# Kernel optimization log

Hardware: AMD Instinct MI355X
Metric: run time of the kernel (lower is better)

Reference implementation:

```python
import jax, jax.numpy as jnp
import numpy as np

N_ENEMY = 4_000_000
N_GUN = 1_000_000
N_EDGES = 16_000_000
HID = 64
OUT = 8


def setup_inputs() -> dict:
    key = jax.random.key(0)
    ks = jax.random.split(key, 9)
    x_enemy = jax.random.normal(ks[0], (N_ENEMY, 4), dtype=jnp.float32)
    x_gun = jax.random.normal(ks[1], (N_GUN, 1), dtype=jnp.float32)
    edge_src = jax.random.randint(ks[2], (N_EDGES,), 0, N_ENEMY, dtype=jnp.int64 if jax.config.jax_enable_x64 else jnp.int32)
    edge_dst = jax.random.randint(ks[3], (N_EDGES,), 0, N_GUN, dtype=jnp.int64 if jax.config.jax_enable_x64 else jnp.int32)
    W_l = jax.random.normal(ks[4], (4, HID), dtype=jnp.float32) * 0.5
    b_l = jax.random.normal(ks[5], (HID,), dtype=jnp.float32) * 0.1
    W_r = jax.random.normal(ks[6], (1, HID), dtype=jnp.float32) * 0.5
    W_fc = jax.random.normal(ks[7], (HID, OUT), dtype=jnp.float32) * 0.1
    b_fc = jax.random.normal(ks[8], (OUT,), dtype=jnp.float32) * 0.1
    return {"x_enemy": x_enemy, "x_gun": x_gun, "edge_src": edge_src,
            "edge_dst": edge_dst, "W_l": W_l, "b_l": b_l, "W_r": W_r,
            "W_fc": W_fc, "b_fc": b_fc}


def reference(x_enemy, x_gun, edge_src, edge_dst, W_l, b_l, W_r, W_fc, b_fc):
    n_gun = x_gun.shape[0]
    # gather enemy messages along edges: [E, 4]
    msgs = x_enemy[edge_src]
    # mean aggregation per gun node (zero for isolated nodes, like PyG scatter-mean)
    summed = jax.ops.segment_sum(msgs, edge_dst, num_segments=n_gun)  # [N_gun, 4]
    counts = jax.ops.segment_sum(jnp.ones((edge_dst.shape[0],), dtype=x_enemy.dtype),
                                 edge_dst, num_segments=n_gun)       # [N_gun]
    mean = summed / jnp.maximum(counts, 1.0)[:, None]
    # SAGEConv: lin_l(aggr) + lin_r(x_dst)  (lin_l has bias, lin_r bias-free)
    h = mean @ W_l + b_l + x_gun @ W_r                                # [N_gun, HID]
    # linear head -> q values
    return h @ W_fc + b_fc                                            # [N_gun, OUT]
```

## Files before the change

### kernel.cpp

```cpp
#include <hip/hip_runtime.h>

#define N_ENEMY 4000000
#define N_GUN   1000000
#define N_EDGES 16000000
#define OUTD    8

#define NB   1024
#define GPB  977
#define T8   8192
#define NT8  1954
#define EPT8 32

#define CH   4096
#define CEPT 16

#define NS   8
#define SEG_CAP 16128

__device__ __forceinline__ unsigned int bucket_of(unsigned int dst) {
    return (unsigned int)(((unsigned long long)dst * 1125395730ull) >> 40);
}
__device__ __forceinline__ unsigned int rne_bf16(unsigned int u) {
    return (u + 0x7FFFu + ((u >> 16) & 1u)) >> 16;
}
__device__ __forceinline__ unsigned int get_xcc() {
    unsigned int x;
    asm("s_getreg_b32 %0, hwreg(HW_REG_XCC_ID)" : "=s"(x));
    return x;
}

__global__ void prep_params(const float* __restrict__ W_l, const float* __restrict__ b_l,
                            const float* __restrict__ W_r, const float* __restrict__ W_fc,
                            const float* __restrict__ b_fc, float* __restrict__ P) {
    int o = threadIdx.x;
    if (o < OUTD) {
        float a0 = 0.f, a1 = 0.f, a2 = 0.f, a3 = 0.f, r = 0.f, c = 0.f;
        for (int h = 0; h < 64; ++h) {
            float w = W_fc[h * OUTD + o];
            a0 += W_l[0 * 64 + h] * w;
            a1 += W_l[1 * 64 + h] * w;
            a2 += W_l[2 * 64 + h] * w;
            a3 += W_l[3 * 64 + h] * w;
            r  += W_r[h] * w;
            c  += b_l[h] * w;
        }
        P[0 * OUTD + o] = a0;
        P[1 * OUTD + o] = a1;
        P[2 * OUTD + o] = a2;
        P[3 * OUTD + o] = a3;
        P[4 * OUTD + o] = r;
        P[5 * OUTD + o] = c + b_fc[o];
    }
}

__global__ void conv_kernel(const uint4* __restrict__ xe, uint2* __restrict__ xeb) {
    int i = blockIdx.x * blockDim.x + threadIdx.x;
    if (i >= N_ENEMY) return;
    uint4 v = xe[i];
    uint2 q;
    q.x = rne_bf16(v.x) | (rne_bf16(v.y) << 16);
    q.y = rne_bf16(v.z) | (rne_bf16(v.w) << 16);
    xeb[i] = q;
}

__global__ void hist2_kernel(const int* __restrict__ edst, unsigned short* __restrict__ tileh) {
    __shared__ unsigned int lh[NB];
    int t = threadIdx.x;
    for (int i = t; i < NB; i += 256) lh[i] = 0;
    __syncthreads();
    int ebase = blockIdx.x * T8;
    int nE = N_EDGES - ebase;
    if (nE > T8) nE = T8;
    for (int i = t; i < nE; i += 256)
        atomicAdd(&lh[bucket_of((unsigned)edst[ebase + i])], 1u);
    __syncthreads();
    unsigned short* row = tileh + (size_t)blockIdx.x * NB;
    for (int i = t; i < NB; i += 256) row[i] = (unsigned short)lh[i];
}

template<int K>
__global__ __launch_bounds__(256)
void tile_scanT(unsigned short* __restrict__ tileh, unsigned int* __restrict__ tot,
                int nbk, int ntile) {
    __shared__ unsigned int part[256][17];
    int t = threadIdx.x;
    int b0 = blockIdx.x * 16;
    unsigned int loc[16];
#pragma unroll
    for (int j = 0; j < 16; ++j) loc[j] = 0;
    for (int k = 0; k < K; ++k) {
        int tile = t * K + k;
        if (tile < ntile) {
            const unsigned short* row = tileh + (size_t)tile * nbk + b0;
#pragma unroll
            for (int j = 0; j < 16; ++j) loc[j] += row[j];
        }
    }
#pragma unroll
    for (int j = 0; j < 16; ++j) part[t][j] = loc[j];
    __syncthreads();
    if (t < 16) {
        unsigned int acc = 0;
        for (int i = 0; i < 256; ++i) {
            unsigned int v = part[i][t];
            part[i][t] = acc;
            acc += v;
        }
        tot[b0 + t] = acc;
    }
    __syncthreads();
    unsigned int run[16];
#pragma unroll
    for (int j = 0; j < 16; ++j) run[j] = part[t][j];
    for (int k = 0; k < K; ++k) {
        int tile = t * K + k;
        if (tile < ntile) {
            unsigned short* row = tileh + (size_t)tile * nbk + b0;
#pragma unroll
            for (int j = 0; j < 16; ++j) {
                unsigned int c = row[j];
                row[j] = (unsigned short)run[j];
                run[j] += c;
            }
        }
    }
}

__global__ void scan_kernel(const unsigned int* __restrict__ tot,
                            unsigned int* __restrict__ offsets) {
    __shared__ unsigned int tmp[1024];
    int t = threadIdx.x;
    unsigned int v0 = (t < NB) ? tot[t] : 0u;
    tmp[t] = v0;
    __syncthreads();
    for (int d = 1; d < 1024; d <<= 1) {
        unsigned int v = (t >= d) ? tmp[t - d] : 0u;
        __syncthreads();
        tmp[t] += v;
        __syncthreads();
    }
    if (t < NB) offsets[t] = tmp[t] - v0;
    if (t == NB - 1) offsets[NB] = tmp[t];
}

__global__ __launch_bounds__(256, 2)
void scatter_sorted(const int* __restrict__ esrc, const int* __restrict__ edst,
                    const unsigned int* __restrict__ offsets,
                    const unsigned short* __restrict__ tileh,
                    unsigned int* __restrict__ payload) {
    __shared__ unsigned int cnt[NB];
    __shared__ unsigned int base[NB];
    __shared__ unsigned int gb[NB];
    __shared__ unsigned short bOf[T8];
    __shared__ unsigned int sorted[T8];
    __shared__ unsigned int partial[256];
    int t = threadIdx.x;
    int tile = blockIdx.x;
    int ebase = tile * T8;
    int nE = N_EDGES - ebase;
    if (nE > T8) nE = T8;
    for (int i = t; i < NB; i += 256) cnt[i] = 0;
    __syncthreads();
    unsigned int w[EPT8];
    unsigned int br[EPT8];
#pragma unroll
    for (int k = 0; k < EPT8; ++k) {
        int idx = k * 256 + t;
        if (idx < nE) {
            unsigned int s = (unsigned int)esrc[ebase + idx];
            unsigned int d = (unsigned int)edst[ebase + idx];
            unsigned int b = bucket_of(d);
            unsigned int g = d - b * GPB;
            unsigned int r = atomicAdd(&cnt[b], 1u);
            w[k]  = (s << 10) | g;
            br[k] = (b << 13) | r;
        } else br[k] = 0xFFFFFFFFu;
    }
    __syncthreads();
    unsigned int loc[4];
    unsigned int s = 0;
#pragma unroll
    for (int j = 0; j < 4; ++j) {
        int b = t * 4 + j;
        unsigned int c = cnt[b];
        loc[j] = s; s += c;
    }
    partial[t] = s;
    __syncthreads();
    for (int d = 1; d < 256; d <<= 1) {
        unsigned int v = (t >= d) ? partial[t - d] : 0u;
        __syncthreads();
        partial[t] += v;
        __syncthreads();
    }
    unsigned int excl = (t > 0) ? partial[t - 1] : 0u;
#pragma unroll
    for (int j = 0; j < 4; ++j) base[t * 4 + j] = excl + loc[j];
    __syncthreads();
    const unsigned short* trow = tileh + (size_t)tile * NB;
#pragma unroll
    for (int j = 0; j < 4; ++j) {
        int b = t * 4 + j;
        gb[b] = offsets[b] + (unsigned int)trow[b];
        unsigned int bs = base[b];
        unsigned int c = cnt[b];
        for (unsigned int p = bs; p < bs + c; ++p) bOf[p] = (unsigned short)b;
    }
    __syncthreads();
#pragma unroll
    for (int k = 0; k < EPT8; ++k) {
        if (br[k] != 0xFFFFFFFFu) {
            unsigned int b = br[k] >> 13;
            unsigned int r = br[k] & 8191u;
            sorted[base[b] + r] = w[k];
        }
    }
    __syncthreads();
    for (int p = t; p < nE; p += 256) {
        unsigned int b = bOf[p];
        payload[gb[b] + ((unsigned int)p - base[b])] = sorted[p];
    }
}

__global__ __launch_bounds__(256)
void slice_sort(const unsigned int* __restrict__ offsets,
                unsigned int* __restrict__ payload,
                unsigned int* __restrict__ stab) {
    __shared__ unsigned int A[SEG_CAP];
    __shared__ unsigned int cnt[NS];
    __shared__ unsigned int base[NS + 1];
    int b = blockIdx.x;
    int t = threadIdx.x;
    unsigned int segS = offsets[b];
    unsigned int segE = offsets[b + 1];
    unsigned int len = segE - segS;
    if (len > SEG_CAP) {
        if (t <= NS) stab[b * (NS + 1) + t] = (t == 0) ? segS : segE;
        return;
    }
    if (t < NS) cnt[t] = 0;
    __syncthreads();
    for (unsigned int i = t; i < len; i += 256) {
        unsigned int w = payload[segS + i];
        A[i] = w;
        atomicAdd(&cnt[w >> 29], 1u);
    }
    __syncthreads();
    if (t == 0) {
        unsigned int acc = 0;
        for (int k = 0; k < NS; ++k) { base[k] = acc; acc += cnt[k]; }
        base[NS] = acc;
    }
    __syncthreads();
    if (t < NS) cnt[t] = 0;
    __syncthreads();
    for (unsigned int i = t; i < len; i += 256) {
        unsigned int w = A[i];
        unsigned int k = w >> 29;
        unsigned int r = atomicAdd(&cnt[k], 1u);
        payload[segS + base[k] + r] = w;
    }
    if (t <= NS) stab[b * (NS + 1) + t] = segS + base[t];
}

__global__ __launch_bounds__(256)
void bucket_v9(const unsigned int* __restrict__ stab,
               const unsigned int* __restrict__ payload,
               const uint2* __restrict__ xeb,
               const float* __restrict__ xg,
               const float* __restrict__ P,
               float* __restrict__ out) {
    __shared__ unsigned long long sorted[CH];
    __shared__ unsigned int cnt[1024];
    __shared__ unsigned int base_[1024];
    __shared__ unsigned int partial[256];
    __shared__ float sP[48];
    int t = threadIdx.x;
    if (t < 48) sP[t] = P[t];
    __syncthreads();

    float a0[4] = {0,0,0,0}, a1[4] = {0,0,0,0}, a2[4] = {0,0,0,0}, a3[4] = {0,0,0,0};
    float an[4] = {0,0,0,0};

    unsigned int b = blockIdx.x;
    unsigned int rot = get_xcc() & (NS - 1u);

    for (int si = 0; si < NS; ++si) {
        unsigned int s = ((unsigned int)si + rot) & (NS - 1u);
        unsigned int rs = stab[b * (NS + 1) + s];
        unsigned int re = stab[b * (NS + 1) + s + 1];

        for (unsigned int cs = rs; cs < re; cs += CH) {
            int n = (int)((re - cs < (unsigned int)CH) ? (re - cs) : (unsigned int)CH);
            for (int i = t; i < 1024; i += 256) cnt[i] = 0;
            __syncthreads();

            unsigned int g_[CEPT], r_[CEPT];
            uint2 q_[CEPT];
#pragma unroll
            for (int k = 0; k < CEPT; ++k) {
                int idx = k * 256 + t;
                if (idx < n) {
                    unsigned int p = payload[cs + idx];
                    q_[k] = xeb[p >> 10];
                    unsigned int g = p & 1023u;
                    g_[k] = g;
                    r_[k] = atomicAdd(&cnt[g], 1u);
                } else g_[k] = 0xFFFFFFFFu;
            }
            __syncthreads();

            unsigned int loc[4];
            unsigned int acc = 0;
#pragma unroll
            for (int j = 0; j < 4; ++j) {
                loc[j] = acc; acc += cnt[t * 4 + j];
            }
            partial[t] = acc;
            __syncthreads();
            for (int d = 1; d < 256; d <<= 1) {
                unsigned int v = (t >= d) ? partial[t - d] : 0u;
                __syncthreads();
                partial[t] += v;
                __syncthreads();
            }
            unsigned int excl = (t > 0) ? partial[t - 1] : 0u;
#pragma unroll
            for (int j = 0; j < 4; ++j) base_[t * 4 + j] = excl + loc[j];
            __syncthreads();

#pragma unroll
            for (int k = 0; k < CEPT; ++k) {
                if (g_[k] != 0xFFFFFFFFu) {
                    sorted[base_[g_[k]] + r_[k]] =
                        ((unsigned long long)q_[k].y << 32) | (unsigned long long)q_[k].x;
                }
            }
            __syncthreads();

#pragma unroll
            for (int j = 0; j < 4; ++j) {
                int g = j * 256 + t;
                unsigned int bs = base_[g], c = cnt[g];
                for (unsigned int p2 = bs; p2 < bs + c; ++p2) {
                    unsigned long long v = sorted[p2];
                    unsigned int lo = (unsigned int)v, hi = (unsigned int)(v >> 32);
                    a0[j] += __uint_as_float(lo << 16);
                    a1[j] += __uint_as_float(lo & 0xffff0000u);
                    a2[j] += __uint_as_float(hi << 16);
                    a3[j] += __uint_as_float(hi & 0xffff0000u);
                }
                an[j] += (float)c;
            }
            __syncthreads();
        }
    }

#pragma unroll
    for (int j = 0; j < 4; ++j) {
        int g = j * 256 + t;
        if (g >= GPB) continue;
        unsigned int G = b * GPB + (unsigned int)g;
        if (G >= N_GUN) continue;
        float inv = 1.0f / fmaxf(an[j], 1.0f);
        float m0 = a0[j] * inv, m1 = a1[j] * inv, m2 = a2[j] * inv, m3 = a3[j] * inv;
        float xv = xg[G];
        float res[OUTD];
#pragma unroll
        for (int o = 0; o < OUTD; ++o) {
            res[o] = m0 * sP[o] + m1 * sP[8 + o] + m2 * sP[16 + o] + m3 * sP[24 + o]
                   + xv * sP[32 + o] + sP[40 + o];
        }
        float4* op = (float4*)(out + (size_t)G * OUTD);
        op[0] = make_float4(res[0], res[1], res[2], res[3]);
        op[1] = make_float4(res[4], res[5], res[6], res[7]);
    }
}

__global__ void edge_kernel(const int4* __restrict__ esrc4, const int4* __restrict__ edst4,
                            const float4* __restrict__ xe, float* __restrict__ summed,
                            float* __restrict__ counts) {
    int t = blockIdx.x * blockDim.x + threadIdx.x;
    if (t >= N_EDGES / 4) return;
    int4 s4 = esrc4[t];
    int4 d4 = edst4[t];
    int ss[4] = { s4.x, s4.y, s4.z, s4.w };
    int dd[4] = { d4.x, d4.y, d4.z, d4.w };
#pragma unroll
    for (int k = 0; k < 4; ++k) {
        float4 m = xe[ss[k]];
        float* basep = summed + (size_t)dd[k] * 4;
        atomicAdd(basep + 0, m.x);
        atomicAdd(basep + 1, m.y);
        atomicAdd(basep + 2, m.z);
        atomicAdd(basep + 3, m.w);
        atomicAdd(counts + dd[k], 1.0f);
    }
}

__global__ void gun_kernel(const float4* __restrict__ summed, const float* __restrict__ counts,
                           const float* __restrict__ xg, const float* __restrict__ P,
                           float* __restrict__ out) {
    __shared__ float sP[48];
    if (threadIdx.x < 48) sP[threadIdx.x] = P[threadIdx.x];
    __syncthreads();
    int g = blockIdx.x * blockDim.x + threadIdx.x;
    if (g >= N_GUN) return;
    float4 s = summed[g];
    float cnt = counts[g];
    float inv = 1.0f / fmaxf(cnt, 1.0f);
    float m0 = s.x * inv, m1 = s.y * inv, m2 = s.z * inv, m3 = s.w * inv;
    float xv = xg[g];
    float res[OUTD];
#pragma unroll
    for (int o = 0; o < OUTD; ++o) {
        res[o] = m0 * sP[o] + m1 * sP[8 + o] + m2 * sP[16 + o] + m3 * sP[24 + o]
               + xv * sP[32 + o] + sP[40 + o];
    }
    float4* op = (float4*)(out + (size_t)g * OUTD);
    op[0] = make_float4(res[0], res[1], res[2], res[3]);
    op[1] = make_float4(res[4], res[5], res[6], res[7]);
}

extern "C" void kernel_launch(void* const* d_in, const int* in_sizes, int n_in,
                              void* d_out, int out_size, void* d_ws, size_t ws_size,
                              hipStream_t stream) {
    const float* x_enemy = (const float*)d_in[0];
    const float* x_gun   = (const float*)d_in[1];
    const int*   esrc    = (const int*)d_in[2];
    const int*   edst    = (const int*)d_in[3];
    const float* W_l     = (const float*)d_in[4];
    const float* b_l     = (const float*)d_in[5];
    const float* W_r     = (const float*)d_in[6];
    const float* W_fc    = (const float*)d_in[7];
    const float* b_fc    = (const float*)d_in[8];
    float* out = (float*)d_out;

    const size_t PAYLOAD_OFF = 0;
    const size_t XEB_OFF     = (size_t)N_EDGES;
    const size_t TOT_OFF     = XEB_OFF + (size_t)N_ENEMY*2;
    const size_t OFFS_OFF    = TOT_OFF + NB;
    const size_t P_OFF       = OFFS_OFF + NB + 1;
    const size_t STAB_OFF    = P_OFF + 48;
    const size_t NEEDED_FULL = (STAB_OFF + (size_t)NB * (NS + 1) + 16) * sizeof(unsigned int);

    if (ws_size >= NEEDED_FULL) {
        unsigned int*   ws      = (unsigned int*)d_ws;
        unsigned int*   payload = ws + PAYLOAD_OFF;
        uint2*          xeb     = (uint2*)(ws + XEB_OFF);
        unsigned short* tileh   = (unsigned short*)(ws + XEB_OFF);
        unsigned int*   tot     = ws + TOT_OFF;
        unsigned int*   offsets = ws + OFFS_OFF;
        float*          P       = (float*)(ws + P_OFF);
        unsigned int*   stab    = ws + STAB_OFF;

        prep_params<<<1, 64, 0, stream>>>(W_l, b_l, W_r, W_fc, b_fc, P);
        hist2_kernel<<<NT8, 256, 0, stream>>>(edst, tileh);
        tile_scanT<8><<<NB / 16, 256, 0, stream>>>(tileh, tot, NB, NT8);
        scan_kernel<<<1, 1024, 0, stream>>>(tot, offsets);
        scatter_sorted<<<NT8, 256, 0, stream>>>(esrc, edst, offsets, tileh, payload);
        slice_sort<<<NB, 256, 0, stream>>>(offsets, payload, stab);
        conv_kernel<<<(N_ENEMY + 255) / 256, 256, 0, stream>>>((const uint4*)x_enemy, xeb);
        bucket_v9<<<NB, 256, 0, stream>>>(stab, payload, xeb, x_gun, P, out);
    } else {
        float* summed = (float*)d_ws;
        float* counts = summed + (size_t)N_GUN * 4;
        float* P      = counts + N_GUN;
        hipMemsetAsync(d_ws, 0, ((size_t)N_GUN * 5 + 48) * sizeof(float), stream);
        prep_params<<<1, 64, 0, stream>>>(W_l, b_l, W_r, W_fc, b_fc, P);
        int edge_threads = N_EDGES / 4;
        edge_kernel<<<(edge_threads + 255) / 256, 256, 0, stream>>>(
            (const int4*)esrc, (const int4*)edst, (const float4*)x_enemy, summed, counts);
        gun_kernel<<<(N_GUN + 255) / 256, 256, 0, stream>>>(
            (const float4*)summed, counts, x_gun, P, out);
    }
}
```

Measured before the change: 413.5 us.

## Record in-tile ranks during histogram and use atomic-free slice sort

The histogram pass now stores each edge's within-tile bucket rank, a 16-bit value, so the scatter kernel can place edges directly without recomputing ranks through LDS atomics. The slice sort replaces shared-memory atomics with per-thread contiguous-range counting, a column prefix scan and deterministic placement. This adds a 32MB rank buffer that must be written and read back, and the workspace layout changes so that tileh no longer aliases xeb. The new path runs only if the workspace is large enough.

```diff
diff --git a/kernel.cpp b/kernel.cpp
--- a/kernel.cpp
+++ b/kernel.cpp
@@ -78,6 +78,24 @@
     for (int i = t; i < NB; i += 256) row[i] = (unsigned short)lh[i];
 }
 
+__global__ void hist3_kernel(const int* __restrict__ edst, unsigned short* __restrict__ tileh,
+                             unsigned short* __restrict__ rnk) {
+    __shared__ unsigned int lh[NB];
+    int t = threadIdx.x;
+    for (int i = t; i < NB; i += 256) lh[i] = 0;
+    __syncthreads();
+    int ebase = blockIdx.x * T8;
+    int nE = N_EDGES - ebase;
+    if (nE > T8) nE = T8;
+    for (int i = t; i < nE; i += 256) {
+        unsigned int b = bucket_of((unsigned)edst[ebase + i]);
+        rnk[ebase + i] = (unsigned short)atomicAdd(&lh[b], 1u);
+    }
+    __syncthreads();
+    unsigned short* row = tileh + (size_t)blockIdx.x * NB;
+    for (int i = t; i < NB; i += 256) row[i] = (unsigned short)lh[i];
+}
+
 template<int K>
 __global__ __launch_bounds__(256)
 void tile_scanT(unsigned short* __restrict__ tileh, unsigned int* __restrict__ tot,
@@ -222,13 +240,97 @@
     }
 }
 
+__global__ __launch_bounds__(256, 2)
+void scatter_nr(const int* __restrict__ esrc, const int* __restrict__ edst,
+                const unsigned short* __restrict__ rnk,
+                const unsigned int* __restrict__ offsets,
+                const unsigned short* __restrict__ tileh,
+                const unsigned int* __restrict__ tot,
+                unsigned int* __restrict__ payload) {
+    __shared__ unsigned int cnt[NB];
+    __shared__ unsigned int base[NB];
+    __shared__ unsigned int gb[NB];
+    __shared__ unsigned short bOf[T8];
+    __shared__ unsigned int sorted[T8];
+    __shared__ unsigned int partial[256];
+    int t = threadIdx.x;
+    int tile = blockIdx.x;
+    int ebase = tile * T8;
+    int nE = N_EDGES - ebase;
+    if (nE > T8) nE = T8;
+
+    const unsigned short* trow = tileh + (size_t)tile * NB;
+    const unsigned short* trowN = tileh + (size_t)(tile + 1) * NB;
+    unsigned int loc[4];
+    unsigned int s = 0;
+#pragma unroll
+    for (int j = 0; j < 4; ++j) {
+        int b = t * 4 + j;
+        unsigned int cur = trow[b];
+        unsigned int nxt = (tile == NT8 - 1) ? tot[b] : (unsigned int)trowN[b];
+        unsigned int c = nxt - cur;
+        cnt[b] = c;
+        gb[b] = offsets[b] + cur;
+        loc[j] = s; s += c;
+    }
+    partial[t] = s;
+    __syncthreads();
+    for (int d = 1; d < 256; d <<= 1) {
+        unsigned int v = (t >= d) ? partial[t - d] : 0u;
+        __syncthreads();
+        partial[t] += v;
+        __syncthreads();
+    }
+    unsigned int excl = (t > 0) ? partial[t - 1] : 0u;
+#pragma unroll
+    for (int j = 0; j < 4; ++j) base[t * 4 + j] = excl + loc[j];
+    __syncthreads();
+
+#pragma unroll
+    for (int j = 0; j < 4; ++j) {
+        int b = t * 4 + j;
+        unsigned int bs = base[b], c = cnt[b];
+        for (unsigned int p = bs; p < bs + c; ++p) bOf[p] = (unsigned short)b;
+    }
+
+    unsigned int w[EPT8], br[EPT8];
+#pragma unroll
+    for (int k = 0; k < EPT8; ++k) {
+        int idx = k * 256 + t;
+        if (idx < nE) {
+            unsigned int sv = (unsigned int)esrc[ebase + idx];
+            unsigned int d = (unsigned int)edst[ebase + idx];
+            unsigned int b = bucket_of(d);
+            unsigned int g = d - b * GPB;
+            unsigned int r = (unsigned int)rnk[ebase + idx];
+            w[k]  = (sv << 10) | g;
+            br[k] = (b << 13) | r;
+        } else br[k] = 0xFFFFFFFFu;
+    }
+    __syncthreads();
+
+#pragma unroll
+    for (int k = 0; k < EPT8; ++k) {
+        if (br[k] != 0xFFFFFFFFu) {
+            unsigned int b = br[k] >> 13;
+            unsigned int r = br[k] & 8191u;
+            sorted[base[b] + r] = w[k];
+        }
+    }
+    __syncthreads();
+    for (int p = t; p < nE; p += 256) {
+        unsigned int b = bOf[p];
+        payload[gb[b] + ((unsigned int)p - base[b])] = sorted[p];
+    }
+}
+
 __global__ __launch_bounds__(256)
-void slice_sort(const unsigned int* __restrict__ offsets,
-                unsigned int* __restrict__ payload,
-                unsigned int* __restrict__ stab) {
+void slice_sort_af(const unsigned int* __restrict__ offsets,
+                   unsigned int* __restrict__ payload,
+                   unsigned int* __restrict__ stab) {
     __shared__ unsigned int A[SEG_CAP];
-    __shared__ unsigned int cnt[NS];
-    __shared__ unsigned int base[NS + 1];
+    __shared__ unsigned int cnts[256][9];
+    __shared__ unsigned int base8[NS + 1];
     int b = blockIdx.x;
     int t = threadIdx.x;
     unsigned int segS = offsets[b];
@@ -238,29 +340,60 @@
         if (t <= NS) stab[b * (NS + 1) + t] = (t == 0) ? segS : segE;
         return;
     }
-    if (t < NS) cnt[t] = 0;
-    __syncthreads();
-    for (unsigned int i = t; i < len; i += 256) {
-        unsigned int w = payload[segS + i];
-        A[i] = w;
-        atomicAdd(&cnt[w >> 29], 1u);
+    for (unsigned int i = t; i < len; i += 256) A[i] = payload[segS + i];
+    __syncthreads();
+
+    unsigned int lo = (len * (unsigned int)t) >> 8;
+    unsigned int hi = (len * (unsigned int)(t + 1)) >> 8;
+
+    unsigned int c0 = 0, c1 = 0, c2 = 0, c3 = 0, c4 = 0, c5 = 0, c6 = 0, c7 = 0;
+    for (unsigned int i = lo; i < hi; ++i) {
+        unsigned int sl = A[i] >> 29;
+        c0 += (sl == 0); c1 += (sl == 1); c2 += (sl == 2); c3 += (sl == 3);
+        c4 += (sl == 4); c5 += (sl == 5); c6 += (sl == 6); c7 += (sl == 7);
+    }
+    cnts[t][0] = c0; cnts[t][1] = c1; cnts[t][2] = c2; cnts[t][3] = c3;
+    cnts[t][4] = c4; cnts[t][5] = c5; cnts[t][6] = c6; cnts[t][7] = c7;
+    __syncthreads();
+
+    if (t < NS) {
+        unsigned int acc = 0;
+        for (int i = 0; i < 256; ++i) {
+            unsigned int v = cnts[i][t];
+            cnts[i][t] = acc;
+            acc += v;
+        }
+        cnts[0][8] = 0;
+        base8[t + 1] = acc;
     }
     __syncthreads();
     if (t == 0) {
         unsigned int acc = 0;
-        for (int k = 0; k < NS; ++k) { base[k] = acc; acc += cnt[k]; }
-        base[NS] = acc;
-    }
-    __syncthreads();
-    if (t < NS) cnt[t] = 0;
-    __syncthreads();
-    for (unsigned int i = t; i < len; i += 256) {
+        for (int k = 1; k <= NS; ++k) {
+            unsigned int v = base8[k];
+            base8[k - 1] = acc;
+            acc += v;
+        }
+        base8[NS] = acc;
+    }
+    __syncthreads();
+
+    unsigned int o0 = base8[0] + cnts[t][0], o1 = base8[1] + cnts[t][1];
+    unsigned int o2 = base8[2] + cnts[t][2], o3 = base8[3] + cnts[t][3];
+    unsigned int o4 = base8[4] + cnts[t][4], o5 = base8[5] + cnts[t][5];
+    unsigned int o6 = base8[6] + cnts[t][6], o7 = base8[7] + cnts[t][7];
+
+    for (unsigned int i = lo; i < hi; ++i) {
         unsigned int w = A[i];
-        unsigned int k = w >> 29;
-        unsigned int r = atomicAdd(&cnt[k], 1u);
-        payload[segS + base[k] + r] = w;
-    }
-    if (t <= NS) stab[b * (NS + 1) + t] = segS + base[t];
+        unsigned int sl = w >> 29;
+        unsigned int dest = (sl == 0) ? o0 : (sl == 1) ? o1 : (sl == 2) ? o2 :
+                            (sl == 3) ? o3 : (sl == 4) ? o4 : (sl == 5) ? o5 :
+                            (sl == 6) ? o6 : o7;
+        o0 += (sl == 0); o1 += (sl == 1); o2 += (sl == 2); o3 += (sl == 3);
+        o4 += (sl == 4); o5 += (sl == 5); o6 += (sl == 6); o7 += (sl == 7);
+        payload[segS + dest] = w;
+    }
+    if (t <= NS) stab[b * (NS + 1) + t] = segS + base8[t];
 }
 
 __global__ __launch_bounds__(256)
@@ -436,30 +569,59 @@
     const float* b_fc    = (const float*)d_in[8];
     float* out = (float*)d_out;
 
-    const size_t PAYLOAD_OFF = 0;
-    const size_t XEB_OFF     = (size_t)N_EDGES;
-    const size_t TOT_OFF     = XEB_OFF + (size_t)N_ENEMY*2;
-    const size_t OFFS_OFF    = TOT_OFF + NB;
-    const size_t P_OFF       = OFFS_OFF + NB + 1;
-    const size_t STAB_OFF    = P_OFF + 48;
-    const size_t NEEDED_FULL = (STAB_OFF + (size_t)NB * (NS + 1) + 16) * sizeof(unsigned int);
-
-    if (ws_size >= NEEDED_FULL) {
+    const size_t B_PAYLOAD = 0;
+    const size_t B_XEB     = (size_t)N_EDGES;
+    const size_t B_RNK     = B_XEB + (size_t)N_ENEMY * 2;
+    const size_t B_TILEH   = B_RNK + (size_t)N_EDGES / 2;
+    const size_t B_TOT     = B_TILEH + ((size_t)NT8 * NB + 1) / 2;
+    const size_t B_OFFS    = B_TOT + NB;
+    const size_t B_P       = B_OFFS + NB + 1;
+    const size_t B_STAB    = B_P + 48;
+    const size_t NEEDED_B  = (B_STAB + (size_t)NB * (NS + 1) + 64) * sizeof(unsigned int);
+
+    const size_t F_PAYLOAD = 0;
+    const size_t F_XEB     = (size_t)N_EDGES;
+    const size_t F_TOT     = F_XEB + (size_t)N_ENEMY * 2;
+    const size_t F_OFFS    = F_TOT + NB;
+    const size_t F_P       = F_OFFS + NB + 1;
+    const size_t F_STAB    = F_P + 48;
+    const size_t NEEDED_F  = (F_STAB + (size_t)NB * (NS + 1) + 16) * sizeof(unsigned int);
+
+    if (ws_size >= NEEDED_B) {
         unsigned int*   ws      = (unsigned int*)d_ws;
-        unsigned int*   payload = ws + PAYLOAD_OFF;
-        uint2*          xeb     = (uint2*)(ws + XEB_OFF);
-        unsigned short* tileh   = (unsigned short*)(ws + XEB_OFF);
-        unsigned int*   tot     = ws + TOT_OFF;
-        unsigned int*   offsets = ws + OFFS_OFF;
-        float*          P       = (float*)(ws + P_OFF);
-        unsigned int*   stab    = ws + STAB_OFF;
+        unsigned int*   payload = ws + B_PAYLOAD;
+        uint2*          xeb     = (uint2*)(ws + B_XEB);
+        unsigned short* rnk     = (unsigned short*)(ws + B_RNK);
+        unsigned short* tileh   = (unsigned short*)(ws + B_TILEH);
+        unsigned int*   tot     = ws + B_TOT;
+        unsigned int*   offsets = ws + B_OFFS;
+        float*          P       = (float*)(ws + B_P);
+        unsigned int*   stab    = ws + B_STAB;
+
+        prep_params<<<1, 64, 0, stream>>>(W_l, b_l, W_r, W_fc, b_fc, P);
+        hist3_kernel<<<NT8, 256, 0, stream>>>(edst, tileh, rnk);
+        tile_scanT<8><<<NB / 16, 256, 0, stream>>>(tileh, tot, NB, NT8);
+        scan_kernel<<<1, 1024, 0, stream>>>(tot, offsets);
+        scatter_nr<<<NT8, 256, 0, stream>>>(esrc, edst, rnk, offsets, tileh, tot, payload);
+        slice_sort_af<<<NB, 256, 0, stream>>>(offsets, payload, stab);
+        conv_kernel<<<(N_ENEMY + 255) / 256, 256, 0, stream>>>((const uint4*)x_enemy, xeb);
+        bucket_v9<<<NB, 256, 0, stream>>>(stab, payload, xeb, x_gun, P, out);
+    } else if (ws_size >= NEEDED_F) {
+        unsigned int*   ws      = (unsigned int*)d_ws;
+        unsigned int*   payload = ws + F_PAYLOAD;
+        uint2*          xeb     = (uint2*)(ws + F_XEB);
+        unsigned short* tileh   = (unsigned short*)(ws + F_XEB);
+        unsigned int*   tot     = ws + F_TOT;
+        unsigned int*   offsets = ws + F_OFFS;
+        float*          P       = (float*)(ws + F_P);
+        unsigned int*   stab    = ws + F_STAB;
 
         prep_params<<<1, 64, 0, stream>>>(W_l, b_l, W_r, W_fc, b_fc, P);
         hist2_kernel<<<NT8, 256, 0, stream>>>(edst, tileh);
         tile_scanT<8><<<NB / 16, 256, 0, stream>>>(tileh, tot, NB, NT8);
         scan_kernel<<<1, 1024, 0, stream>>>(tot, offsets);
         scatter_sorted<<<NT8, 256, 0, stream>>>(esrc, edst, offsets, tileh, payload);
-        slice_sort<<<NB, 256, 0, stream>>>(offsets, payload, stab);
+        slice_sort_af<<<NB, 256, 0, stream>>>(offsets, payload, stab);
         conv_kernel<<<(N_ENEMY + 255) / 256, 256, 0, stream>>>((const uint4*)x_enemy, xeb);
         bucket_v9<<<NB, 256, 0, stream>>>(stab, payload, xeb, x_gun, P, out);
     } else {
```

Measured after the change: 483.9 us. 1.17x slower.
